# Performance work log

Measured on AMD Instinct MI355X. Metric: run time of the kernel, lower is better.

## Reference

```python
import jax, jax.numpy as jnp
import numpy as np

H = 2048          # hidden_size
NQ = 16           # num_q_heads
NKV = 4           # num_kv_heads
HD = H // NQ      # head_dim = 128
REP = NQ // NKV   # kv repeat factor
FF = 8192         # intermediate_size
B, S = 2, 2048
EPS = 1e-6


def setup_inputs() -> dict:
    key = jax.random.key(0)
    ks = jax.random.split(key, 12)
    sd = 0.02
    return {
        "hidden_states": jax.random.normal(ks[0], (B, S, H), jnp.float32),
        "Wq": jax.random.normal(ks[1], (H, H), jnp.float32) * sd,
        "bq": jnp.zeros((H,), jnp.float32),
        "Wk": jax.random.normal(ks[2], (H, NKV * HD), jnp.float32) * sd,
        "bk": jnp.zeros((NKV * HD,), jnp.float32),
        "Wv": jax.random.normal(ks[3], (H, NKV * HD), jnp.float32) * sd,
        "bv": jnp.zeros((NKV * HD,), jnp.float32),
        "Wo": jax.random.normal(ks[4], (H, H), jnp.float32) * sd,
        "bo": jnp.zeros((H,), jnp.float32),
        "W1": jax.random.normal(ks[5], (H, FF), jnp.float32) * sd,
        "b1": jnp.zeros((FF,), jnp.float32),
        "W2": jax.random.normal(ks[6], (FF, H), jnp.float32) * sd,
        "b2": jnp.zeros((H,), jnp.float32),
        "g1": jnp.ones((H,), jnp.float32),  # ln1 weight
        "g2": jnp.ones((H,), jnp.float32),  # ln2 weight
    }


def _rmsnorm(x, g):
    rms = jnp.sqrt(jnp.mean(x * x, axis=-1, keepdims=True) + EPS)
    return g * (x / rms)


def _attention(x, Wq, bq, Wk, bk, Wv, bv, Wo, bo):
    b, s, _ = x.shape
    q = (x @ Wq + bq).reshape(b, s, NQ, HD).transpose(0, 2, 1, 3)    # [b,hq,s,d]
    k = (x @ Wk + bk).reshape(b, s, NKV, HD).transpose(0, 2, 1, 3)   # [b,hkv,s,d]
    v = (x @ Wv + bv).reshape(b, s, NKV, HD).transpose(0, 2, 1, 3)
    k = jnp.repeat(k, REP, axis=1)  # GQA: repeat_interleave over head dim
    v = jnp.repeat(v, REP, axis=1)
    scale = 1.0 / np.sqrt(HD).astype(np.float32)
    scores = jnp.einsum("bhqd,bhkd->bhqk", q, k) * scale
    causal = jnp.triu(jnp.ones((s, s), bool), k=1)                   # True above diag
    scores = jnp.where(causal[None, None], -jnp.inf, scores)
    probs = jax.nn.softmax(scores, axis=-1)
    ctx = jnp.einsum("bhqk,bhkd->bhqd", probs, v)
    ctx = ctx.transpose(0, 2, 1, 3).reshape(b, s, H)
    return ctx @ Wo + bo


def reference(hidden_states, Wq, bq, Wk, bk, Wv, bv, Wo, bo, W1, b1, W2, b2, g1, g2):
    x = hidden_states
    # pre-norm attention block
    x = x + _attention(_rmsnorm(x, g1), Wq, bq, Wk, bk, Wv, bv, Wo, bo)
    # pre-norm FFN block (exact GELU, matching torch nn.GELU default)
    h = _rmsnorm(x, g2)
    h = jax.nn.gelu(h @ W1 + b1, approximate=False) @ W2 + b2
    return x + h
```

## Files before the change

kernel.cpp:

```cpp
#include <hip/hip_runtime.h>
#include <cstdint>

#define H_    2048
#define NQ_   16
#define NKV_  4
#define HD_   128
#define FF_   8192
#define B_    2
#define S_    2048
#define TOK   (B_*S_)
#define QKVN  (H_ + 2*NKV_*HD_)
#define KVB   64

typedef __bf16 bf16;
typedef bf16  bf16x8 __attribute__((ext_vector_type(8)));
typedef float f32x4  __attribute__((ext_vector_type(4)));

typedef __attribute__((address_space(1))) void as1_void;
typedef __attribute__((address_space(3))) void as3_void;

__device__ __forceinline__ void gload_lds16(const void* g, void* l) {
    __builtin_amdgcn_global_load_lds((as1_void*)g, (as3_void*)l, 16, 0, 0);
}

__global__ __launch_bounds__(256) void wtrans_kernel(
    const float* __restrict__ W, bf16* __restrict__ Wt, int K, int N, int outOff)
{
    __shared__ float tile[32][33];
    const int n0 = (int)blockIdx.x * 32;
    const int k0 = (int)blockIdx.y * 32;
    const int c  = (int)threadIdx.x & 31;
    const int r  = (int)threadIdx.x >> 5;
#pragma unroll
    for (int i = 0; i < 4; ++i)
        tile[r + i*8][c] = W[(size_t)(k0 + r + i*8) * N + n0 + c];
    __syncthreads();
#pragma unroll
    for (int i = 0; i < 4; ++i)
        Wt[(size_t)(outOff + n0 + r + i*8) * K + k0 + c] = (bf16)tile[c][r + i*8];
}

__global__ void biaspack_kernel(const float* __restrict__ bq, const float* __restrict__ bk,
                                const float* __restrict__ bv, float* __restrict__ out)
{
    const int i = (int)(blockIdx.x * 256 + threadIdx.x);
    out[i] = (i < H_) ? bq[i] : (i < H_ + NKV_*HD_ ? bk[i - H_] : bv[i - H_ - NKV_*HD_]);
}

__global__ __launch_bounds__(256) void rmsnorm_kernel(
    const float* __restrict__ x, const float* __restrict__ g, bf16* __restrict__ y)
{
    const int row = (int)blockIdx.x;
    const int tid = (int)threadIdx.x;
    const float* xr = x + (size_t)row * H_;
    const float4 a = *(const float4*)(xr + tid*8);
    const float4 c = *(const float4*)(xr + tid*8 + 4);
    float ss = a.x*a.x + a.y*a.y + a.z*a.z + a.w*a.w
             + c.x*c.x + c.y*c.y + c.z*c.z + c.w*c.w;
#pragma unroll
    for (int d = 1; d < 64; d <<= 1) ss += __shfl_xor(ss, d);
    __shared__ float red[4];
    if ((tid & 63) == 0) red[tid >> 6] = ss;
    __syncthreads();
    const float inv = rsqrtf((red[0]+red[1]+red[2]+red[3]) * (1.0f/H_) + 1e-6f);
    const float vals[8] = {a.x,a.y,a.z,a.w,c.x,c.y,c.z,c.w};
    const float* gp = g + tid*8;
    bf16x8 outv;
#pragma unroll
    for (int e = 0; e < 8; ++e) outv[e] = (bf16)(vals[e] * inv * gp[e]);
    *(bf16x8*)(y + (size_t)row * H_ + tid*8) = outv;
}

__global__ __launch_bounds__(256) void vtrans_kernel(
    const bf16* __restrict__ qkv, bf16* __restrict__ Vt)
{
    __shared__ bf16 tile[32][33];
    const int tt = (int)blockIdx.x;
    const int d0 = (int)blockIdx.y * 32;
    const int kh = (int)blockIdx.z;
    const int b  = (tt*32) / S_;
    const int s0 = (tt*32) % S_;
    const int c = (int)threadIdx.x & 31;
    const int r = (int)threadIdx.x >> 5;
#pragma unroll
    for (int i = 0; i < 4; ++i)
        tile[r + i*8][c] = qkv[(size_t)(tt*32 + r + i*8)*QKVN + H_ + NKV_*HD_ + kh*HD_ + d0 + c];
    __syncthreads();
#pragma unroll
    for (int i = 0; i < 4; ++i)
        Vt[((size_t)(b*NKV_ + kh)*HD_ + d0 + r + i*8)*S_ + s0 + c] = tile[c][r + i*8];
}

template<int MODE>
__global__ __launch_bounds__(256, 3) void gemm_kernel(
    const bf16* __restrict__ A, const bf16* __restrict__ Bt,
    const float* __restrict__ bias, const float* __restrict__ resid,
    void* __restrict__ Cout, int M, int N, int K)
{
    __shared__ bf16 lA[128*64];
    __shared__ bf16 lB[128*64];
    const int tid  = (int)threadIdx.x;
    const int wid  = tid >> 6;
    const int lane = tid & 63;
    const int lr   = lane & 15;
    const int lg   = lane >> 4;

    const int gx  = (int)gridDim.x;
    const int nwg = gx * (int)gridDim.y;
    int wg = (int)blockIdx.y * gx + (int)blockIdx.x;
    wg = (wg & 7) * (nwg >> 3) + (wg >> 3);
    const int nsup  = gx >> 2;
    const int chunk = wg >> 5;
    const int cin   = wg & 31;
    const int m0 = ((chunk / nsup) * 8 + (cin >> 2)) * 128;
    const int n0 = ((chunk % nsup) * 4 + (cin & 3)) * 128;

    const int wm = (wid >> 1) * 64;
    const int wn = (wid & 1) * 64;

    f32x4 acc[4][4] = {};

    const int sRow = wid*32 + (lane >> 3);
    const int sCol = ((lane & 7) ^ (lane >> 3)) * 8;
    const bf16* aSrc = A  + (size_t)(m0 + sRow) * K + sCol;
    const bf16* bSrc = Bt + (size_t)(n0 + sRow) * K + sCol;

    for (int k0 = 0; k0 < K; k0 += 64) {
#pragma unroll
        for (int i = 0; i < 4; ++i) {
            gload_lds16(aSrc + (size_t)(i*8)*K + k0, &lA[(wid*32 + i*8)*64]);
            gload_lds16(bSrc + (size_t)(i*8)*K + k0, &lB[(wid*32 + i*8)*64]);
        }
        __syncthreads();
#pragma unroll
        for (int kk = 0; kk < 64; kk += 32) {
            const int ks = (kk + lg*8) ^ ((lr & 7) * 8);
            bf16x8 af[4], bfr[4];
#pragma unroll
            for (int i = 0; i < 4; ++i)
                af[i] = *(const bf16x8*)&lA[(wm + i*16 + lr)*64 + ks];
#pragma unroll
            for (int j = 0; j < 4; ++j)
                bfr[j] = *(const bf16x8*)&lB[(wn + j*16 + lr)*64 + ks];
#pragma unroll
            for (int i = 0; i < 4; ++i)
#pragma unroll
                for (int j = 0; j < 4; ++j)
                    acc[i][j] = __builtin_amdgcn_mfma_f32_16x16x32_bf16(
                        af[i], bfr[j], acc[i][j], 0, 0, 0);
        }
        __syncthreads();
    }

#pragma unroll
    for (int j = 0; j < 4; ++j) {
        const int col = n0 + wn + j*16 + lr;
        const float bj = bias[col];
#pragma unroll
        for (int i = 0; i < 4; ++i) {
            const int row0 = m0 + wm + i*16 + lg*4;
#pragma unroll
            for (int rr = 0; rr < 4; ++rr) {
                float v = acc[i][j][rr] + bj;
                const size_t idx = (size_t)(row0 + rr) * N + col;
                if (MODE == 2) {
                    ((float*)Cout)[idx] = v + resid[idx];
                } else {
                    if (MODE == 1) v = 0.5f * v * (1.0f + erff(v * 0.70710678118654752f));
                    ((bf16*)Cout)[idx] = (bf16)v;
                }
            }
        }
    }
}

__global__ __launch_bounds__(256) void attn_kernel(
    const bf16* __restrict__ qkv, const bf16* __restrict__ Vt,
    bf16* __restrict__ ctx)
{
    __shared__ bf16 lK[2][KVB*HD_];
    __shared__ bf16 lV[2][HD_*KVB];
    __shared__ bf16 lP[4][16*72];
    const int tid  = (int)threadIdx.x;
    const int wid  = tid >> 6;
    const int lane = tid & 63;
    const int lr   = lane & 15;
    const int lg   = lane >> 4;
    const int qt = (int)gridDim.x - 1 - (int)blockIdx.x;
    const int h = (int)blockIdx.y, b = (int)blockIdx.z;
    const int kh = h >> 2;
    const int qb = qt * 64;
    const int qw = qb + wid * 16;
    const float scale = 0.08838834764831845f;

    const bf16* kB[4];
    const bf16* vB[4];
#pragma unroll
    for (int i = 0; i < 4; ++i) {
        const int kRow = (wid*4 + i)*4 + (lane >> 4);
        const int kCol = ((lane & 15) ^ (kRow & 7)) * 8;
        kB[i] = qkv + (size_t)(b*S_ + kRow)*QKVN + H_ + kh*HD_ + kCol;
        const int vRow = (wid*4 + i)*8 + (lane >> 3);
        const int vCol = ((lane & 7) ^ (vRow & 7)) * 8;
        vB[i] = Vt + ((size_t)(b*NKV_ + kh)*HD_ + vRow)*S_ + vCol;
    }

    bf16x8 qf[4];
    {
        const bf16* qp = qkv + (size_t)(b*S_ + qw + lr)*QKVN + h*HD_ + lg*8;
#pragma unroll
        for (int t = 0; t < 4; ++t) qf[t] = *(const bf16x8*)(qp + t*32);
    }

    f32x4 o[8] = {};
    float mrow[4] = {-__builtin_inff(), -__builtin_inff(), -__builtin_inff(), -__builtin_inff()};
    float lrow[4] = {0.f, 0.f, 0.f, 0.f};
    const int nt = qt + 1;

#pragma unroll
    for (int i = 0; i < 4; ++i) {
        gload_lds16(kB[i], &lK[0][(wid*4 + i)*4*HD_]);
        gload_lds16(vB[i], &lV[0][(wid*4 + i)*8*KVB]);
    }

    int cur = 0;
    for (int t = 0; t < nt; ++t) {
        __syncthreads();
        if (t + 1 < nt) {
            const size_t kAdd = (size_t)(t+1)*KVB*QKVN;
            const size_t vAdd = (size_t)(t+1)*KVB;
#pragma unroll
            for (int i = 0; i < 4; ++i) {
                gload_lds16(kB[i] + kAdd, &lK[cur^1][(wid*4 + i)*4*HD_]);
                gload_lds16(vB[i] + vAdd, &lV[cur^1][(wid*4 + i)*8*KVB]);
            }
        }
        const int kv0 = t * KVB;

        f32x4 s[4] = {};
#pragma unroll
        for (int sub = 0; sub < 4; ++sub) {
            const int krow = sub*16 + lr;
            const bf16* kr = &lK[cur][krow*HD_];
            const int swk = (krow & 7) * 8;
#pragma unroll
            for (int d = 0; d < 4; ++d) {
                const bf16x8 kf = *(const bf16x8*)(kr + ((d*32 + lg*8) ^ swk));
                s[sub] = __builtin_amdgcn_mfma_f32_16x16x32_bf16(qf[d], kf, s[sub], 0, 0, 0);
            }
        }

        float p[4][4], rmax[4];
        if (t == qt) {
#pragma unroll
            for (int rr = 0; rr < 4; ++rr) {
                const int q = qw + lg*4 + rr;
                rmax[rr] = -__builtin_inff();
#pragma unroll
                for (int sub = 0; sub < 4; ++sub) {
                    const int kv = kv0 + sub*16 + lr;
                    const float v = s[sub][rr] * scale;
                    p[sub][rr] = (kv <= q) ? v : -__builtin_inff();
                    rmax[rr] = fmaxf(rmax[rr], p[sub][rr]);
                }
            }
        } else {
#pragma unroll
            for (int rr = 0; rr < 4; ++rr) {
                rmax[rr] = -__builtin_inff();
#pragma unroll
                for (int sub = 0; sub < 4; ++sub) {
                    p[sub][rr] = s[sub][rr] * scale;
                    rmax[rr] = fmaxf(rmax[rr], p[sub][rr]);
                }
            }
        }
#pragma unroll
        for (int d = 1; d < 16; d <<= 1)
#pragma unroll
            for (int rr = 0; rr < 4; ++rr)
                rmax[rr] = fmaxf(rmax[rr], __shfl_xor(rmax[rr], d));

        float fsc[4], rsum[4];
#pragma unroll
        for (int rr = 0; rr < 4; ++rr) {
            const float mn = fmaxf(mrow[rr], rmax[rr]);
            fsc[rr]  = __expf(mrow[rr] - mn);
            mrow[rr] = mn;
            rsum[rr] = 0.f;
#pragma unroll
            for (int sub = 0; sub < 4; ++sub) {
                p[sub][rr] = __expf(p[sub][rr] - mn);
                rsum[rr] += p[sub][rr];
            }
        }
#pragma unroll
        for (int d = 1; d < 16; d <<= 1)
#pragma unroll
            for (int rr = 0; rr < 4; ++rr)
                rsum[rr] += __shfl_xor(rsum[rr], d);
#pragma unroll
        for (int rr = 0; rr < 4; ++rr) lrow[rr] = lrow[rr]*fsc[rr] + rsum[rr];
#pragma unroll
        for (int dch = 0; dch < 8; ++dch)
#pragma unroll
            for (int rr = 0; rr < 4; ++rr) o[dch][rr] *= fsc[rr];

#pragma unroll
        for (int sub = 0; sub < 4; ++sub)
#pragma unroll
            for (int rr = 0; rr < 4; ++rr)
                lP[wid][(lg*4 + rr)*72 + sub*16 + lr] = (bf16)p[sub][rr];
        bf16x8 pfr[2];
#pragma unroll
        for (int kk = 0; kk < 2; ++kk)
            pfr[kk] = *(const bf16x8*)&lP[wid][lr*72 + kk*32 + lg*8];

#pragma unroll
        for (int dch = 0; dch < 8; ++dch) {
            const bf16* vr = &lV[cur][(dch*16 + lr)*KVB];
            const int swv = (lr & 7) * 8;
#pragma unroll
            for (int kk = 0; kk < 2; ++kk) {
                const bf16x8 vf = *(const bf16x8*)(vr + ((kk*32 + lg*8) ^ swv));
                o[dch] = __builtin_amdgcn_mfma_f32_16x16x32_bf16(pfr[kk], vf, o[dch], 0, 0, 0);
            }
        }
        cur ^= 1;
    }

#pragma unroll
    for (int rr = 0; rr < 4; ++rr) {
        const float inv = 1.0f / lrow[rr];
        bf16* cp = ctx + (size_t)(b*S_ + qw + lg*4 + rr) * H_ + h*HD_ + lr;
#pragma unroll
        for (int dch = 0; dch < 8; ++dch)
            cp[dch*16] = (bf16)(o[dch][rr] * inv);
    }
}

extern "C" void kernel_launch(void* const* d_in, const int* in_sizes, int n_in,
                              void* d_out, int out_size, void* d_ws, size_t ws_size,
                              hipStream_t stream)
{
    const float* hidden = (const float*)d_in[0];
    const float* Wq = (const float*)d_in[1];
    const float* bq = (const float*)d_in[2];
    const float* Wk = (const float*)d_in[3];
    const float* bk = (const float*)d_in[4];
    const float* Wv = (const float*)d_in[5];
    const float* bv = (const float*)d_in[6];
    const float* Wo = (const float*)d_in[7];
    const float* bo = (const float*)d_in[8];
    const float* W1 = (const float*)d_in[9];
    const float* b1 = (const float*)d_in[10];
    const float* W2 = (const float*)d_in[11];
    const float* b2 = (const float*)d_in[12];
    const float* g1 = (const float*)d_in[13];
    const float* g2 = (const float*)d_in[14];
    float* out = (float*)d_out;

    char* p = (char*)d_ws;
    auto alloc = [&](size_t bytes) { char* r = p; p += (bytes + 255) & ~(size_t)255; return r; };
    bf16*  wt_qkv = (bf16*)alloc((size_t)QKVN * H_ * 2);
    bf16*  wo_t   = (bf16*)alloc((size_t)H_ * H_ * 2);
    bf16*  w1_t   = (bf16*)alloc((size_t)FF_ * H_ * 2);
    bf16*  w2_t   = (bf16*)alloc((size_t)H_ * FF_ * 2);
    float* bqkv   = (float*)alloc((size_t)QKVN * 4);
    bf16*  xn1    = (bf16*)alloc((size_t)TOK * H_ * 2);
    bf16*  qkv    = (bf16*)alloc((size_t)TOK * QKVN * 2);
    bf16*  ctxb   = (bf16*)alloc((size_t)TOK * H_ * 2);
    float* x1     = (float*)alloc((size_t)TOK * H_ * 4);
    bf16*  xn2    = (bf16*)alloc((size_t)TOK * H_ * 2);
    bf16*  ffn    = (bf16*)alloc((size_t)TOK * FF_ * 2);
    bf16*  vt     = xn1;

    const dim3 blk(256);
    biaspack_kernel<<<dim3(QKVN/256), blk, 0, stream>>>(bq, bk, bv, bqkv);
    wtrans_kernel<<<dim3(H_/32,  H_/32),  blk, 0, stream>>>(Wq, wt_qkv, H_, H_,  0);
    wtrans_kernel<<<dim3(512/32, H_/32),  blk, 0, stream>>>(Wk, wt_qkv, H_, 512, H_);
    wtrans_kernel<<<dim3(512/32, H_/32),  blk, 0, stream>>>(Wv, wt_qkv, H_, 512, H_ + 512);
    wtrans_kernel<<<dim3(H_/32,  H_/32),  blk, 0, stream>>>(Wo, wo_t,   H_, H_,  0);
    wtrans_kernel<<<dim3(FF_/32, H_/32),  blk, 0, stream>>>(W1, w1_t,   H_, FF_, 0);
    wtrans_kernel<<<dim3(H_/32,  FF_/32), blk, 0, stream>>>(W2, w2_t,   FF_, H_, 0);

    rmsnorm_kernel<<<dim3(TOK), blk, 0, stream>>>(hidden, g1, xn1);
    gemm_kernel<0><<<dim3(QKVN/128, TOK/128), blk, 0, stream>>>(
        xn1, wt_qkv, bqkv, nullptr, qkv, TOK, QKVN, H_);
    vtrans_kernel<<<dim3(TOK/32, HD_/32, NKV_), blk, 0, stream>>>(qkv, vt);
    attn_kernel<<<dim3(S_/64, NQ_, B_), blk, 0, stream>>>(qkv, vt, ctxb);
    gemm_kernel<2><<<dim3(H_/128, TOK/128), blk, 0, stream>>>(
        ctxb, wo_t, bo, hidden, x1, TOK, H_, H_);
    rmsnorm_kernel<<<dim3(TOK), blk, 0, stream>>>(x1, g2, xn2);
    gemm_kernel<1><<<dim3(FF_/128, TOK/128), blk, 0, stream>>>(
        xn2, w1_t, b1, nullptr, ffn, TOK, FF_, H_);
    gemm_kernel<2><<<dim3(H_/128, TOK/128), blk, 0, stream>>>(
        ffn, w2_t, b2, x1, out, TOK, H_, FF_);
}
```

Baseline: 732.3 us.

## Double attention query tile per block and stagger GEMM K-loop start

Result: slower. 977.2 us (+33.4%).

```diff
diff --git a/kernel.cpp b/kernel.cpp
--- a/kernel.cpp
+++ b/kernel.cpp
@@ -125,7 +125,11 @@
     const bf16* aSrc = A  + (size_t)(m0 + sRow) * K + sCol;
     const bf16* bSrc = Bt + (size_t)(n0 + sRow) * K + sCol;
 
-    for (int k0 = 0; k0 < K; k0 += 64) {
+    const int NT = K >> 6;
+    int kt = (int)((((unsigned)wg * 2654435761u) >> 16) & (unsigned)(NT - 1));
+
+    for (int t = 0; t < NT; ++t) {
+        const size_t k0 = (size_t)kt << 6;
 #pragma unroll
         for (int i = 0; i < 4; ++i) {
             gload_lds16(aSrc + (size_t)(i*8)*K + k0, &lA[(wid*32 + i*8)*64]);
@@ -150,6 +154,7 @@
                         af[i], bfr[j], acc[i][j], 0, 0, 0);
         }
         __syncthreads();
+        kt = (kt + 1 == NT) ? 0 : kt + 1;
     }
 
 #pragma unroll
@@ -186,11 +191,11 @@
     const int lane = tid & 63;
     const int lr   = lane & 15;
     const int lg   = lane >> 4;
-    const int qt = (int)gridDim.x - 1 - (int)blockIdx.x;
+    const int qtb = (int)gridDim.x - 1 - (int)blockIdx.x;
     const int h = (int)blockIdx.y, b = (int)blockIdx.z;
     const int kh = h >> 2;
-    const int qb = qt * 64;
-    const int qw = qb + wid * 16;
+    const int qb = qtb * 128;
+    const int qw0 = qb + wid * 32;
     const float scale = 0.08838834764831845f;
 
     const bf16* kB[4];
@@ -205,17 +210,21 @@
         vB[i] = Vt + ((size_t)(b*NKV_ + kh)*HD_ + vRow)*S_ + vCol;
     }
 
-    bf16x8 qf[4];
-    {
-        const bf16* qp = qkv + (size_t)(b*S_ + qw + lr)*QKVN + h*HD_ + lg*8;
-#pragma unroll
-        for (int t = 0; t < 4; ++t) qf[t] = *(const bf16x8*)(qp + t*32);
-    }
-
-    f32x4 o[8] = {};
-    float mrow[4] = {-__builtin_inff(), -__builtin_inff(), -__builtin_inff(), -__builtin_inff()};
-    float lrow[4] = {0.f, 0.f, 0.f, 0.f};
-    const int nt = qt + 1;
+    bf16x8 qf[2][4];
+#pragma unroll
+    for (int s = 0; s < 2; ++s) {
+        const bf16* qp = qkv + (size_t)(b*S_ + qw0 + s*16 + lr)*QKVN + h*HD_ + lg*8;
+#pragma unroll
+        for (int t4 = 0; t4 < 4; ++t4) qf[s][t4] = *(const bf16x8*)(qp + t4*32);
+    }
+
+    f32x4 o[2][8] = {};
+    float mrow[2][4], lrow[2][4];
+#pragma unroll
+    for (int s = 0; s < 2; ++s)
+#pragma unroll
+        for (int rr = 0; rr < 4; ++rr) { mrow[s][rr] = -__builtin_inff(); lrow[s][rr] = 0.f; }
+    const int nt = qtb*2 + 2;
 
 #pragma unroll
     for (int i = 0; i < 4; ++i) {
@@ -237,106 +246,113 @@
         }
         const int kv0 = t * KVB;
 
-        f32x4 s[4] = {};
-#pragma unroll
-        for (int sub = 0; sub < 4; ++sub) {
-            const int krow = sub*16 + lr;
-            const bf16* kr = &lK[cur][krow*HD_];
-            const int swk = (krow & 7) * 8;
-#pragma unroll
-            for (int d = 0; d < 4; ++d) {
-                const bf16x8 kf = *(const bf16x8*)(kr + ((d*32 + lg*8) ^ swk));
-                s[sub] = __builtin_amdgcn_mfma_f32_16x16x32_bf16(qf[d], kf, s[sub], 0, 0, 0);
-            }
-        }
-
-        float p[4][4], rmax[4];
-        if (t == qt) {
+#pragma unroll
+        for (int s = 0; s < 2; ++s) {
+            const int qws = qw0 + s*16;
+
+            f32x4 sc[4] = {};
+#pragma unroll
+            for (int sub = 0; sub < 4; ++sub) {
+                const int krow = sub*16 + lr;
+                const bf16* kr = &lK[cur][krow*HD_];
+                const int swk = (krow & 7) * 8;
+#pragma unroll
+                for (int d = 0; d < 4; ++d) {
+                    const bf16x8 kf = *(const bf16x8*)(kr + ((d*32 + lg*8) ^ swk));
+                    sc[sub] = __builtin_amdgcn_mfma_f32_16x16x32_bf16(qf[s][d], kf, sc[sub], 0, 0, 0);
+                }
+            }
+
+            float p[4][4], rmax[4];
+            if (kv0 + KVB - 1 > qws) {
+#pragma unroll
+                for (int rr = 0; rr < 4; ++rr) {
+                    const int q = qws + lg*4 + rr;
+                    rmax[rr] = -__builtin_inff();
+#pragma unroll
+                    for (int sub = 0; sub < 4; ++sub) {
+                        const int kv = kv0 + sub*16 + lr;
+                        const float v = sc[sub][rr] * scale;
+                        p[sub][rr] = (kv <= q) ? v : -__builtin_inff();
+                        rmax[rr] = fmaxf(rmax[rr], p[sub][rr]);
+                    }
+                }
+            } else {
+#pragma unroll
+                for (int rr = 0; rr < 4; ++rr) {
+                    rmax[rr] = -__builtin_inff();
+#pragma unroll
+                    for (int sub = 0; sub < 4; ++sub) {
+                        p[sub][rr] = sc[sub][rr] * scale;
+                        rmax[rr] = fmaxf(rmax[rr], p[sub][rr]);
+                    }
+                }
+            }
+#pragma unroll
+            for (int d = 1; d < 16; d <<= 1)
+#pragma unroll
+                for (int rr = 0; rr < 4; ++rr)
+                    rmax[rr] = fmaxf(rmax[rr], __shfl_xor(rmax[rr], d));
+
+            float fsc[4], rsum[4];
 #pragma unroll
             for (int rr = 0; rr < 4; ++rr) {
-                const int q = qw + lg*4 + rr;
-                rmax[rr] = -__builtin_inff();
+                const float mn = fmaxf(mrow[s][rr], rmax[rr]);
+                fsc[rr]  = __expf(mrow[s][rr] - mn);
+                mrow[s][rr] = mn;
+                rsum[rr] = 0.f;
 #pragma unroll
                 for (int sub = 0; sub < 4; ++sub) {
-                    const int kv = kv0 + sub*16 + lr;
-                    const float v = s[sub][rr] * scale;
-                    p[sub][rr] = (kv <= q) ? v : -__builtin_inff();
-                    rmax[rr] = fmaxf(rmax[rr], p[sub][rr]);
-                }
-            }
-        } else {
-#pragma unroll
-            for (int rr = 0; rr < 4; ++rr) {
-                rmax[rr] = -__builtin_inff();
-#pragma unroll
-                for (int sub = 0; sub < 4; ++sub) {
-                    p[sub][rr] = s[sub][rr] * scale;
-                    rmax[rr] = fmaxf(rmax[rr], p[sub][rr]);
-                }
-            }
-        }
-#pragma unroll
-        for (int d = 1; d < 16; d <<= 1)
-#pragma unroll
-            for (int rr = 0; rr < 4; ++rr)
-                rmax[rr] = fmaxf(rmax[rr], __shfl_xor(rmax[rr], d));
-
-        float fsc[4], rsum[4];
+                    p[sub][rr] = __expf(p[sub][rr] - mn);
+                    rsum[rr] += p[sub][rr];
+                }
+            }
+#pragma unroll
+            for (int d = 1; d < 16; d <<= 1)
+#pragma unroll
+                for (int rr = 0; rr < 4; ++rr)
+                    rsum[rr] += __shfl_xor(rsum[rr], d);
+#pragma unroll
+            for (int rr = 0; rr < 4; ++rr) lrow[s][rr] = lrow[s][rr]*fsc[rr] + rsum[rr];
+#pragma unroll
+            for (int dch = 0; dch < 8; ++dch)
+#pragma unroll
+                for (int rr = 0; rr < 4; ++rr) o[s][dch][rr] *= fsc[rr];
+
+#pragma unroll
+            for (int sub = 0; sub < 4; ++sub)
+#pragma unroll
+                for (int rr = 0; rr < 4; ++rr)
+                    lP[wid][(lg*4 + rr)*72 + sub*16 + lr] = (bf16)p[sub][rr];
+            bf16x8 pfr[2];
+#pragma unroll
+            for (int kk = 0; kk < 2; ++kk)
+                pfr[kk] = *(const bf16x8*)&lP[wid][lr*72 + kk*32 + lg*8];
+
+#pragma unroll
+            for (int dch = 0; dch < 8; ++dch) {
+                const bf16* vr = &lV[cur][(dch*16 + lr)*KVB];
+                const int swv = (lr & 7) * 8;
+#pragma unroll
+                for (int kk = 0; kk < 2; ++kk) {
+                    const bf16x8 vf = *(const bf16x8*)(vr + ((kk*32 + lg*8) ^ swv));
+                    o[s][dch] = __builtin_amdgcn_mfma_f32_16x16x32_bf16(pfr[kk], vf, o[s][dch], 0, 0, 0);
+                }
+            }
+        }
+        cur ^= 1;
+    }
+
+#pragma unroll
+    for (int s = 0; s < 2; ++s)
 #pragma unroll
         for (int rr = 0; rr < 4; ++rr) {
-            const float mn = fmaxf(mrow[rr], rmax[rr]);
-            fsc[rr]  = __expf(mrow[rr] - mn);
-            mrow[rr] = mn;
-            rsum[rr] = 0.f;
-#pragma unroll
-            for (int sub = 0; sub < 4; ++sub) {
-                p[sub][rr] = __expf(p[sub][rr] - mn);
-                rsum[rr] += p[sub][rr];
-            }
-        }
-#pragma unroll
-        for (int d = 1; d < 16; d <<= 1)
-#pragma unroll
-            for (int rr = 0; rr < 4; ++rr)
-                rsum[rr] += __shfl_xor(rsum[rr], d);
-#pragma unroll
-        for (int rr = 0; rr < 4; ++rr) lrow[rr] = lrow[rr]*fsc[rr] + rsum[rr];
-#pragma unroll
-        for (int dch = 0; dch < 8; ++dch)
-#pragma unroll
-            for (int rr = 0; rr < 4; ++rr) o[dch][rr] *= fsc[rr];
-
-#pragma unroll
-        for (int sub = 0; sub < 4; ++sub)
-#pragma unroll
-            for (int rr = 0; rr < 4; ++rr)
-                lP[wid][(lg*4 + rr)*72 + sub*16 + lr] = (bf16)p[sub][rr];
-        bf16x8 pfr[2];
-#pragma unroll
-        for (int kk = 0; kk < 2; ++kk)
-            pfr[kk] = *(const bf16x8*)&lP[wid][lr*72 + kk*32 + lg*8];
-
-#pragma unroll
-        for (int dch = 0; dch < 8; ++dch) {
-            const bf16* vr = &lV[cur][(dch*16 + lr)*KVB];
-            const int swv = (lr & 7) * 8;
-#pragma unroll
-            for (int kk = 0; kk < 2; ++kk) {
-                const bf16x8 vf = *(const bf16x8*)(vr + ((kk*32 + lg*8) ^ swv));
-                o[dch] = __builtin_amdgcn_mfma_f32_16x16x32_bf16(pfr[kk], vf, o[dch], 0, 0, 0);
-            }
-        }
-        cur ^= 1;
-    }
-
-#pragma unroll
-    for (int rr = 0; rr < 4; ++rr) {
-        const float inv = 1.0f / lrow[rr];
-        bf16* cp = ctx + (size_t)(b*S_ + qw + lg*4 + rr) * H_ + h*HD_ + lr;
-#pragma unroll
-        for (int dch = 0; dch < 8; ++dch)
-            cp[dch*16] = (bf16)(o[dch][rr] * inv);
-    }
+            const float inv = 1.0f / lrow[s][rr];
+            bf16* cp = ctx + (size_t)(b*S_ + qw0 + s*16 + lg*4 + rr) * H_ + h*HD_ + lr;
+#pragma unroll
+            for (int dch = 0; dch < 8; ++dch)
+                cp[dch*16] = (bf16)(o[s][dch][rr] * inv);
+        }
 }
 
 extern "C" void kernel_launch(void* const* d_in, const int* in_sizes, int n_in,
@@ -388,7 +404,7 @@
     gemm_kernel<0><<<dim3(QKVN/128, TOK/128), blk, 0, stream>>>(
         xn1, wt_qkv, bqkv, nullptr, qkv, TOK, QKVN, H_);
     vtrans_kernel<<<dim3(TOK/32, HD_/32, NKV_), blk, 0, stream>>>(qkv, vt);
-    attn_kernel<<<dim3(S_/64, NQ_, B_), blk, 0, stream>>>(qkv, vt, ctxb);
+    attn_kernel<<<dim3(S_/128, NQ_, B_), blk, 0, stream>>>(qkv, vt, ctxb);
     gemm_kernel<2><<<dim3(H_/128, TOK/128), blk, 0, stream>>>(
         ctxb, wo_t, bo, hidden, x1, TOK, H_, H_);
     rmsnorm_kernel<<<dim3(TOK), blk, 0, stream>>>(x1, g2, xn2);
```
